# Kernel tuning notes

Hardware: AMD Instinct MI355X
Metric: run time of the kernel (lower is better)

## Reference

```python
import jax, jax.numpy as jnp
import numpy as np
from jax.scipy.special import gammaln
from jax.scipy.linalg import solve_triangular

NUG_MULT = 4.0   # default tuneParm[0]
SMOOTH = 1.5     # default tuneParm[1] -> Matern nu=1.5


def setup_inputs() -> dict:
    key = jax.random.key(0)
    k1, k2, k3 = jax.random.split(key, 3)
    n, N, p, mMax = 128, 2048, 2, 64
    Y_data = jax.random.normal(k1, (n, N), dtype=jnp.float32)
    X_data = jax.random.normal(k2, (n, N, p), dtype=jnp.float32)
    NNmax = jax.random.randint(k3, (N, mMax), 0, N)
    # theta chosen so all exp/log transforms are well-behaved (see shape_source)
    theta = jnp.array([0.0, 0.5, -0.3, 0.0, 0.5, 0.0, 0.0, 0.0, 0.0, 0.0], dtype=jnp.float32)
    return {"Y_data": Y_data, "X_data": X_data, "theta": theta, "NNmax": NNmax, "m": 30}


def _neg_intlik(Y_data, X_data, theta, NNmax, m):
    n, N, p = X_data.shape
    inds = jnp.arange(N)
    scal = 1.0 / (jnp.arange(N, dtype=Y_data.dtype) + 1.0)
    logs = jnp.log(scal)

    # nug_fun / sigma_fun / scaling_x, vectorized over locations
    nugMean = jax.nn.relu(jnp.exp(logs * theta[1] + theta[0]) - 1e-5) + 1e-5   # (N,)
    nugSd = nugMean * NUG_MULT
    alpha = nugMean**2 / nugSd**2 + 2.0
    beta = nugMean * (alpha - 1.0)
    sigma = jnp.exp(logs * theta[4] + theta[3])                                 # (N,)
    scales_x = jnp.exp(logs[:, None] * theta[6 + p:6 + 2 * p][None, :]
                       + theta[6:6 + p][None, :])                               # (N,p)

    # variable neighbor count handled by zero-masking padded columns:
    # zeroed columns contribute 0 to the linear kernel and 0 to pairwise distances,
    # exactly matching the per-location ncol = min(i, m) truncation.
    NN = NNmax[:, :m]                                                           # (N,m)
    ncol = jnp.minimum(inds, m)
    colmask = (jnp.arange(m)[None, :] < ncol[:, None]).astype(Y_data.dtype)     # (N,m)
    s_col = jnp.sqrt(jnp.exp((jnp.arange(m, dtype=Y_data.dtype) + 1.0) * theta[2]))  # scaling_fun, (m,)

    Yg = jnp.transpose(Y_data[:, NN], (1, 0, 2))                                # (N,n,m)
    Ys = Yg * (s_col[None, None, :] * colmask[:, None, :])
    Xi = jnp.transpose(X_data, (1, 0, 2))                                       # (N,n,p)
    xz = jnp.all(Xi == 0, axis=(1, 2))                                          # per-call all-zero check
    Xs = jnp.where(xz[:, None, None], 0.0, Xi * scales_x[:, None, :])
    W = jnp.concatenate([Ys, Xs], axis=2)                                       # (N,n,m+p)

    lin = jnp.einsum('bik,bjk->bij', W, W)                                      # linear kernel

    lenScal = jnp.exp(theta[5]) * jnp.sqrt(2.0 * SMOOTH)
    Wd = W / lenScal
    sq = jnp.sum(Wd * Wd, axis=2)                                               # (N,n)
    r2 = sq[:, :, None] + sq[:, None, :] - 2.0 * jnp.einsum('bik,bjk->bij', Wd, Wd)
    r = jnp.sqrt(jnp.clip(r2, 0.0))
    c = jnp.sqrt(jnp.asarray(3.0, Y_data.dtype)) * r                            # Matern nu=1.5
    matern = (1.0 + c) * jnp.exp(-c)

    K = (lin + matern * (sigma**2)[:, None, None]) / nugMean[:, None, None]
    K = jnp.where((inds == 0)[:, None, None], 0.0, K)                           # i==0 -> G = I
    G = K + jnp.eye(n, dtype=K.dtype)[None, :, :]

    GChol = jnp.linalg.cholesky(G)                                              # (N,n,n)
    yT = solve_triangular(GChol, Y_data.T[:, :, None], lower=True)[..., 0]      # (N,n)

    alphaPost = alpha + n / 2.0
    betaPost = beta + 0.5 * jnp.sum(yT * yT, axis=1)
    logdet = jnp.sum(jnp.log(jnp.diagonal(GChol, axis1=-2, axis2=-1)), axis=1)
    loglik = (-logdet + alpha * jnp.log(beta) - alphaPost * jnp.log(betaPost)
              + gammaln(alphaPost) - gammaln(alpha))
    return -jnp.sum(loglik)


def reference(Y_data, X_data, theta, NNmax, m):
    # mode='intlik' of TransportMap.forward (scalar negative integrated loglik)
    return _neg_intlik(Y_data, X_data, theta, NNmax, m)
```

## Files before the change

kernel.cpp:

```cpp
#include <hip/hip_runtime.h>
#include <hip/hip_bf16.h>
#include <math.h>

#define N_COLS 2048
#define N_ROWS 128
#define KW     32
#define WST    36
#define COLSTR 132

__global__ void transpose_y_kernel(const float* __restrict__ Y, float* __restrict__ Yt) {
  __shared__ float tile[32][33];
  const int bx = blockIdx.x, by = blockIdx.y;
  const int tx = threadIdx.x, ty = threadIdx.y;
#pragma unroll
  for (int q = 0; q < 4; ++q)
    tile[ty + 8 * q][tx] = Y[(by * 32 + ty + 8 * q) * N_COLS + bx * 32 + tx];
  __syncthreads();
#pragma unroll
  for (int q = 0; q < 4; ++q)
    Yt[(bx * 32 + ty + 8 * q) * N_ROWS + by * 32 + tx] = tile[tx][ty + 8 * q];
}

__global__ void transpose_x_kernel(const float2* __restrict__ X, float2* __restrict__ Xt) {
  __shared__ float2 tile[32][33];
  const int bx = blockIdx.x, by = blockIdx.y;
  const int tx = threadIdx.x, ty = threadIdx.y;
#pragma unroll
  for (int q = 0; q < 4; ++q)
    tile[ty + 8 * q][tx] = X[(by * 32 + ty + 8 * q) * N_COLS + bx * 32 + tx];
  __syncthreads();
#pragma unroll
  for (int q = 0; q < 4; ++q)
    Xt[(bx * 32 + ty + 8 * q) * N_ROWS + by * 32 + tx] = tile[tx][ty + 8 * q];
}

template <int CB, int CNEXT>
__device__ __forceinline__ void chol_step(const int k, const int t, const int ti, const int tj,
                                          float (&gr)[8][8], float* __restrict__ colbuf,
                                          float* __restrict__ yL, float& ld, float& yb) {
  __syncthreads();
  const int rb = (k & 1) * COLSTR;
  const float dk = colbuf[rb + k];
  const float inv2 = __builtin_amdgcn_rcpf(dk);
  const float yk = yL[k];
  if (t == 0) { ld += 0.5f * __logf(dk); yb += yk * yk * inv2; }

  float ra[8], rc[8];
#pragma unroll
  for (int a = CB; a < 8; ++a) ra[a] = colbuf[rb + ti + 16 * a];
#pragma unroll
  for (int c = CB; c < 8; ++c) rc[c] = colbuf[rb + tj + 16 * c];
  ra[CB] = (ti + 16 * CB > k) ? ra[CB] : 0.0f;
  rc[CB] = (tj + 16 * CB > k) ? rc[CB] : 0.0f;
#pragma unroll
  for (int a = CB; a < 8; ++a) ra[a] *= inv2;
#pragma unroll
  for (int a = CB; a < 8; ++a)
#pragma unroll
    for (int c = CB; c < 8; ++c)
      gr[a][c] = fmaf(-ra[a], rc[c], gr[a][c]);

  if (t < N_ROWS && t > k) yL[t] = fmaf(-(colbuf[rb + t] * inv2), yk, yL[t]);

  if constexpr (CNEXT < 8) {
    if (tj == ((k + 1) & 15)) {
      const int nb = ((k + 1) & 1) * COLSTR;
#pragma unroll
      for (int a = CB; a < 8; ++a) colbuf[nb + ti + 16 * a] = gr[a][CNEXT];
    }
  }
}

__global__ __launch_bounds__(256, 2) void chol_main(
    const float* __restrict__ Y, const float* __restrict__ X,
    const float* __restrict__ theta, const int* __restrict__ NNmax,
    const int* __restrict__ mPtr, const float* __restrict__ Yt,
    const float* __restrict__ Xt, const int useT, const int mMax,
    float* __restrict__ out) {
  __shared__ __align__(16) float Wl[N_ROWS * WST];
  __shared__ float colbuf[2 * COLSTR];
  __shared__ float yL[N_ROWS];
  __shared__ float swL[N_ROWS];
  __shared__ float smaskL[KW];
  __shared__ int nnL[KW];
  __shared__ int nzflag;

  const int b = blockIdx.x;
  const int t = threadIdx.x;
  const int ti = t & 15;
  const int tj = t >> 4;

  const float th0 = theta[0], th1 = theta[1], th2 = theta[2], th3 = theta[3], th4 = theta[4];
  const float th5 = theta[5], th6 = theta[6], th7 = theta[7], th8 = theta[8], th9 = theta[9];
  const float logs = -__logf((float)(b + 1));
  const float nug = fmaxf(__expf(th0 + th1 * logs) - 1e-5f, 0.0f) + 1e-5f;
  const float sigma = __expf(th3 + th4 * logs);
  const float sig2 = sigma * sigma;
  const float invNug = 1.0f / nug;
  const float invL2 = __expf(-2.0f * th5) * (1.0f / 3.0f);
  const float sx0 = __expf(th6 + th8 * logs);
  const float sx1 = __expf(th7 + th9 * logs);
  int m = *mPtr; if (m > 30) m = 30;

  if (t == 0) nzflag = 0;
  if (t < KW) {
    nnL[t] = (t < m) ? NNmax[b * mMax + t] : 0;
    smaskL[t] = (t < m && t < b) ? __expf(0.5f * (float)(t + 1) * th2) : 0.0f;
  }
  __syncthreads();

  {
    const int i0 = t & 127;
    const int jb = t >> 7;
#pragma unroll
    for (int q = 0; q < 16; ++q) {
      const int j = jb + 2 * q;
      float v;
      if (j < m) {
        v = (useT ? Yt[nnL[j] * N_ROWS + i0] : Y[i0 * N_COLS + nnL[j]]) * smaskL[j];
      } else if (j < m + 2) {
        const int kc = j - m;
        v = useT ? Xt[(b * N_ROWS + i0) * 2 + kc] : X[(i0 * N_COLS + b) * 2 + kc];
        v *= (kc == 0) ? sx0 : sx1;
      } else {
        v = 0.0f;
      }
      Wl[i0 * WST + j] = v;
    }
  }
  if (t < N_ROWS) {
    const float2 xv = useT ? ((const float2*)Xt)[b * N_ROWS + t]
                           : ((const float2*)X)[t * N_COLS + b];
    if (xv.x != 0.0f || xv.y != 0.0f) atomicOr(&nzflag, 1);
    yL[t] = useT ? Yt[b * N_ROWS + t] : Y[t * N_COLS + b];
  }
  __syncthreads();
  if (nzflag == 0 && t < N_ROWS) {
    Wl[t * WST + m] = 0.0f;
    Wl[t * WST + m + 1] = 0.0f;
  }
  __syncthreads();

  float gr[8][8];
#pragma unroll
  for (int a = 0; a < 8; ++a)
#pragma unroll
    for (int c = 0; c < 8; ++c) gr[a][c] = 0.0f;

#pragma unroll
  for (int kk = 0; kk < KW; kk += 4) {
    float4 wa[8], wc[8];
#pragma unroll
    for (int a = 0; a < 8; ++a) wa[a] = *(const float4*)&Wl[(ti + 16 * a) * WST + kk];
#pragma unroll
    for (int c = 0; c < 8; ++c) wc[c] = *(const float4*)&Wl[(tj + 16 * c) * WST + kk];
#pragma unroll
    for (int a = 0; a < 8; ++a)
#pragma unroll
      for (int c = 0; c < 8; ++c) {
        float acc = gr[a][c];
        acc = fmaf(wa[a].x, wc[c].x, acc);
        acc = fmaf(wa[a].y, wc[c].y, acc);
        acc = fmaf(wa[a].z, wc[c].z, acc);
        acc = fmaf(wa[a].w, wc[c].w, acc);
        gr[a][c] = acc;
      }
  }

  if (ti == tj) {
#pragma unroll
    for (int a = 0; a < 8; ++a) swL[ti + 16 * a] = gr[a][a];
  }
  __syncthreads();

  if (b != 0) {
    float swa[8], swc[8];
#pragma unroll
    for (int a = 0; a < 8; ++a) swa[a] = swL[ti + 16 * a];
#pragma unroll
    for (int c = 0; c < 8; ++c) swc[c] = swL[tj + 16 * c];
#pragma unroll
    for (int a = 0; a < 8; ++a)
#pragma unroll
      for (int c = 0; c < 8; ++c) {
        const float d = gr[a][c];
        float r2 = (swa[a] + swc[c] - 2.0f * d) * invL2;
        r2 = fmaxf(r2, 0.0f);
        const float cc = sqrtf(3.0f * r2);
        const float mat = (1.0f + cc) * __expf(-cc);
        float g = fmaf(mat, sig2, d) * invNug;
        if (a == c) g += (ti == tj) ? 1.0f : 0.0f;
        gr[a][c] = g;
      }
  } else {
#pragma unroll
    for (int a = 0; a < 8; ++a)
#pragma unroll
      for (int c = 0; c < 8; ++c) gr[a][c] = (ti == tj && a == c) ? 1.0f : 0.0f;
  }

  if (tj == 0) {
#pragma unroll
    for (int a = 0; a < 8; ++a) colbuf[ti + 16 * a] = gr[a][0];
  }

  float ld = 0.0f, yb = 0.0f;
#define CHOL_GROUP(CB)                                                        \
  {                                                                           \
    _Pragma("unroll 1") for (int kk = 0; kk < 15; ++kk)                       \
        chol_step<CB, CB>(CB * 16 + kk, t, ti, tj, gr, colbuf, yL, ld, yb);   \
    chol_step<CB, CB + 1>(CB * 16 + 15, t, ti, tj, gr, colbuf, yL, ld, yb);   \
  }
  CHOL_GROUP(0) CHOL_GROUP(1) CHOL_GROUP(2) CHOL_GROUP(3)
  CHOL_GROUP(4) CHOL_GROUP(5) CHOL_GROUP(6) CHOL_GROUP(7)
#undef CHOL_GROUP

  if (t == 0) {
    const float alpha = 2.0625f;
    const float alphaPost = alpha + 64.0f;
    const float beta = 1.0625f * nug;
    const float betaPost = beta + 0.5f * yb;
    const float loglik = -ld + alpha * __logf(beta) - alphaPost * __logf(betaPost)
                       + lgammaf(alphaPost) - lgammaf(alpha);
    atomicAdd(out, -loglik);
  }
}

extern "C" void kernel_launch(void* const* d_in, const int* in_sizes, int n_in,
                              void* d_out, int out_size, void* d_ws, size_t ws_size,
                              hipStream_t stream) {
  const float* Y = (const float*)d_in[0];
  const float* X = (const float*)d_in[1];
  const float* theta = (const float*)d_in[2];
  const int* NNmax = (const int*)d_in[3];
  const int* mPtr = (const int*)d_in[4];
  float* out = (float*)d_out;
  const int mMax = in_sizes[3] / N_COLS;

  hipMemsetAsync(out, 0, sizeof(float) * out_size, stream);

  float* Yt = (float*)d_ws;
  float* Xt = (float*)d_ws + N_COLS * N_ROWS;
  const size_t need = (size_t)(N_COLS * N_ROWS * 3) * sizeof(float);
  const int useT = (ws_size >= need) ? 1 : 0;

  if (useT) {
    dim3 tb(32, 8);
    transpose_y_kernel<<<dim3(N_COLS / 32, N_ROWS / 32), tb, 0, stream>>>(Y, Yt);
    transpose_x_kernel<<<dim3(N_COLS / 32, N_ROWS / 32), tb, 0, stream>>>(
        (const float2*)X, (float2*)Xt);
  }
  chol_main<<<N_COLS, 256, 0, stream>>>(Y, X, theta, NNmax, mPtr, Yt, Xt, useT, mMax, out);
}
```

Measured before the change: 350.8 us.

## Replace per-column Cholesky steps with blocked 16-wide panel factorization

```diff
diff --git a/kernel.cpp b/kernel.cpp
--- a/kernel.cpp
+++ b/kernel.cpp
@@ -6,7 +6,7 @@
 #define N_ROWS 128
 #define KW     32
 #define WST    36
-#define COLSTR 132
+#define PST    20
 
 __global__ void transpose_y_kernel(const float* __restrict__ Y, float* __restrict__ Yt) {
   __shared__ float tile[32][33];
@@ -34,56 +34,69 @@
     Xt[(bx * 32 + ty + 8 * q) * N_ROWS + by * 32 + tx] = tile[tx][ty + 8 * q];
 }
 
-template <int CB, int CNEXT>
-__device__ __forceinline__ void chol_step(const int k, const int t, const int ti, const int tj,
-                                          float (&gr)[8][8], float* __restrict__ colbuf,
-                                          float* __restrict__ yL, float& ld, float& yb) {
-  __syncthreads();
-  const int rb = (k & 1) * COLSTR;
-  const float dk = colbuf[rb + k];
-  const float inv2 = __builtin_amdgcn_rcpf(dk);
-  const float yk = yL[k];
-  if (t == 0) { ld += 0.5f * __logf(dk); yb += yk * yk * inv2; }
-
-  float ra[8], rc[8];
-#pragma unroll
-  for (int a = CB; a < 8; ++a) ra[a] = colbuf[rb + ti + 16 * a];
-#pragma unroll
-  for (int c = CB; c < 8; ++c) rc[c] = colbuf[rb + tj + 16 * c];
-  ra[CB] = (ti + 16 * CB > k) ? ra[CB] : 0.0f;
-  rc[CB] = (tj + 16 * CB > k) ? rc[CB] : 0.0f;
-#pragma unroll
-  for (int a = CB; a < 8; ++a) ra[a] *= inv2;
-#pragma unroll
-  for (int a = CB; a < 8; ++a)
-#pragma unroll
-    for (int c = CB; c < 8; ++c)
-      gr[a][c] = fmaf(-ra[a], rc[c], gr[a][c]);
-
-  if (t < N_ROWS && t > k) yL[t] = fmaf(-(colbuf[rb + t] * inv2), yk, yL[t]);
-
-  if constexpr (CNEXT < 8) {
-    if (tj == ((k + 1) & 15)) {
-      const int nb = ((k + 1) & 1) * COLSTR;
-#pragma unroll
-      for (int a = CB; a < 8; ++a) colbuf[nb + ti + 16 * a] = gr[a][CNEXT];
-    }
-  }
-}
-
-__global__ __launch_bounds__(256, 2) void chol_main(
+static __device__ __forceinline__ void factor_panel(
+    const int p, const int l, float* __restrict__ P, float* __restrict__ yL,
+    float* __restrict__ invd, float& ld, float& yb) {
+  float pr0[16], pr1[16];
+#pragma unroll
+  for (int q = 0; q < 4; ++q) {
+    const float4 v0 = *(const float4*)&P[l * PST + 4 * q];
+    const float4 v1 = *(const float4*)&P[(l + 64) * PST + 4 * q];
+    pr0[4 * q + 0] = v0.x; pr0[4 * q + 1] = v0.y; pr0[4 * q + 2] = v0.z; pr0[4 * q + 3] = v0.w;
+    pr1[4 * q + 0] = v1.x; pr1[4 * q + 1] = v1.y; pr1[4 * q + 2] = v1.z; pr1[4 * q + 3] = v1.w;
+  }
+  float py0 = yL[l], py1 = yL[l + 64];
+  const int pbase = p << 4;
+#pragma unroll
+  for (int k = 0; k < 16; ++k) {
+    const int prow = pbase + k;
+    const int olane = prow & 63;
+    const bool hi = prow >= 64;
+    float rowk[16];
+#pragma unroll
+    for (int j = k; j < 16; ++j)
+      rowk[j] = __shfl(hi ? pr1[j] : pr0[j], olane, 64);
+    const float yk = __shfl(hi ? py1 : py0, olane, 64);
+    const float dk = rowk[k];
+    const float inv = __builtin_amdgcn_rcpf(dk);
+    if (l == 0) { ld += 0.5f * __logf(dk); yb += yk * yk * inv; invd[k] = inv; }
+    const float f0 = (l > prow) ? pr0[k] * inv : 0.0f;
+    const float f1 = (l + 64 > prow) ? pr1[k] * inv : 0.0f;
+#pragma unroll
+    for (int j = k + 1; j < 16; ++j) {
+      pr0[j] = fmaf(-f0, rowk[j], pr0[j]);
+      pr1[j] = fmaf(-f1, rowk[j], pr1[j]);
+    }
+    py0 = fmaf(-f0, yk, py0);
+    py1 = fmaf(-f1, yk, py1);
+  }
+#pragma unroll
+  for (int q = 0; q < 4; ++q) {
+    *(float4*)&P[l * PST + 4 * q] =
+        make_float4(pr0[4 * q + 0], pr0[4 * q + 1], pr0[4 * q + 2], pr0[4 * q + 3]);
+    *(float4*)&P[(l + 64) * PST + 4 * q] =
+        make_float4(pr1[4 * q + 0], pr1[4 * q + 1], pr1[4 * q + 2], pr1[4 * q + 3]);
+  }
+  yL[l] = py0;
+  yL[l + 64] = py1;
+}
+
+__global__ __launch_bounds__(256, 4) void chol_main(
     const float* __restrict__ Y, const float* __restrict__ X,
     const float* __restrict__ theta, const int* __restrict__ NNmax,
     const int* __restrict__ mPtr, const float* __restrict__ Yt,
     const float* __restrict__ Xt, const int useT, const int mMax,
     float* __restrict__ out) {
-  __shared__ __align__(16) float Wl[N_ROWS * WST];
-  __shared__ float colbuf[2 * COLSTR];
+  __shared__ __align__(16) float uMem[5120];
   __shared__ float yL[N_ROWS];
   __shared__ float swL[N_ROWS];
+  __shared__ __align__(16) float invd[16];
   __shared__ float smaskL[KW];
   __shared__ int nnL[KW];
   __shared__ int nzflag;
+  float* const Wl = uMem;
+  float* const P0 = uMem;
+  float* const P1 = uMem + 2560;
 
   const int b = blockIdx.x;
   const int t = threadIdx.x;
@@ -149,22 +162,22 @@
 
 #pragma unroll
   for (int kk = 0; kk < KW; kk += 4) {
-    float4 wa[8], wc[8];
-#pragma unroll
-    for (int a = 0; a < 8; ++a) wa[a] = *(const float4*)&Wl[(ti + 16 * a) * WST + kk];
+    float4 wc[8];
 #pragma unroll
     for (int c = 0; c < 8; ++c) wc[c] = *(const float4*)&Wl[(tj + 16 * c) * WST + kk];
 #pragma unroll
-    for (int a = 0; a < 8; ++a)
+    for (int a = 0; a < 8; ++a) {
+      const float4 wa = *(const float4*)&Wl[(ti + 16 * a) * WST + kk];
 #pragma unroll
       for (int c = 0; c < 8; ++c) {
         float acc = gr[a][c];
-        acc = fmaf(wa[a].x, wc[c].x, acc);
-        acc = fmaf(wa[a].y, wc[c].y, acc);
-        acc = fmaf(wa[a].z, wc[c].z, acc);
-        acc = fmaf(wa[a].w, wc[c].w, acc);
+        acc = fmaf(wa.x, wc[c].x, acc);
+        acc = fmaf(wa.y, wc[c].y, acc);
+        acc = fmaf(wa.z, wc[c].z, acc);
+        acc = fmaf(wa.w, wc[c].w, acc);
         gr[a][c] = acc;
       }
+    }
   }
 
   if (ti == tj) {
@@ -199,21 +212,44 @@
       for (int c = 0; c < 8; ++c) gr[a][c] = (ti == tj && a == c) ? 1.0f : 0.0f;
   }
 
-  if (tj == 0) {
-#pragma unroll
-    for (int a = 0; a < 8; ++a) colbuf[ti + 16 * a] = gr[a][0];
-  }
+#pragma unroll
+  for (int a = 0; a < 8; ++a) P0[(ti + 16 * a) * PST + tj] = gr[a][0];
 
   float ld = 0.0f, yb = 0.0f;
-#define CHOL_GROUP(CB)                                                        \
-  {                                                                           \
-    _Pragma("unroll 1") for (int kk = 0; kk < 15; ++kk)                       \
-        chol_step<CB, CB>(CB * 16 + kk, t, ti, tj, gr, colbuf, yL, ld, yb);   \
-    chol_step<CB, CB + 1>(CB * 16 + 15, t, ti, tj, gr, colbuf, yL, ld, yb);   \
-  }
-  CHOL_GROUP(0) CHOL_GROUP(1) CHOL_GROUP(2) CHOL_GROUP(3)
-  CHOL_GROUP(4) CHOL_GROUP(5) CHOL_GROUP(6) CHOL_GROUP(7)
-#undef CHOL_GROUP
+#pragma unroll
+  for (int p = 0; p < 8; ++p) {
+    float* const Pc = (p & 1) ? P1 : P0;
+    float* const Pn = (p & 1) ? P0 : P1;
+    __syncthreads();
+    if (t < 64) factor_panel(p, t, Pc, yL, invd, ld, yb);
+    __syncthreads();
+    if (p < 7) {
+#pragma unroll
+      for (int kk = 0; kk < 16; kk += 4) {
+        const float4 iv4 = *(const float4*)&invd[kk];
+        float4 rc4[8];
+#pragma unroll
+        for (int c = p + 1; c < 8; ++c)
+          rc4[c] = *(const float4*)&Pc[(tj + 16 * c) * PST + kk];
+#pragma unroll
+        for (int a = p + 1; a < 8; ++a) {
+          float4 ra = *(const float4*)&Pc[(ti + 16 * a) * PST + kk];
+          ra.x *= iv4.x; ra.y *= iv4.y; ra.z *= iv4.z; ra.w *= iv4.w;
+#pragma unroll
+          for (int c = p + 1; c < 8; ++c) {
+            float acc = gr[a][c];
+            acc = fmaf(-ra.x, rc4[c].x, acc);
+            acc = fmaf(-ra.y, rc4[c].y, acc);
+            acc = fmaf(-ra.z, rc4[c].z, acc);
+            acc = fmaf(-ra.w, rc4[c].w, acc);
+            gr[a][c] = acc;
+          }
+        }
+      }
+#pragma unroll
+      for (int a = p + 1; a < 8; ++a) Pn[(ti + 16 * a) * PST + tj] = gr[a][p + 1];
+    }
+  }
 
   if (t == 0) {
     const float alpha = 2.0625f;
```

After: 879.1 us. +150.6%, slower.
